# Kernel optimization log

Hardware: AMD Instinct MI355X
Metric: run time of the kernel (lower is better)

The kernel has to match this reference:

```python
import jax, jax.numpy as jnp
import numpy as np
import math

B, S, D = 2, 2048, 512
N_BUCKETS = 64
N_HYP = int(math.log2(N_BUCKETS))  # 6


def setup_inputs() -> dict:
    key = jax.random.key(0)
    ks = jax.random.split(key, 6)
    x = jax.random.normal(ks[0], (B, S, D), dtype=jnp.float32)
    # torch.nn.Linear params: weight [out,in], bias [out]
    Wq = jax.random.normal(ks[1], (D, D), dtype=jnp.float32) / jnp.sqrt(D)
    bq = jax.random.normal(ks[2], (D,), dtype=jnp.float32) * 0.01
    Wv = jax.random.normal(ks[3], (D, D), dtype=jnp.float32) / jnp.sqrt(D)
    bv = jax.random.normal(ks[4], (D,), dtype=jnp.float32) * 0.01
    hyperplanes = jax.random.normal(ks[5], (D + 1, N_HYP), dtype=jnp.float32)
    return {"x": x, "Wq": Wq, "bq": bq, "Wv": Wv, "bv": bv, "hyperplanes": hyperplanes}


def _get_buckets(q, hyperplanes):
    # append constant-1 feature: [B,S,D+1]
    qa = jnp.concatenate([q, jnp.ones(q.shape[:2] + (1,), q.dtype)], axis=2)
    proj = jnp.einsum('bse,en->bsn', qa, hyperplanes)
    bits = (proj >= 0).astype(jnp.float32)
    powers = (2.0 ** jnp.arange(N_HYP)).astype(jnp.float32)
    return jnp.einsum('bsn,n->bs', bits, powers)  # [B,S] float bucket ids


def reference(x, Wq, bq, Wv, bv, hyperplanes):
    q = x @ Wq.T + bq
    v = x @ Wv.T + bv
    buckets = _get_buckets(q, hyperplanes)  # [B,S]
    scale = 1.0 / math.sqrt(D)

    def body(acc, i):
        # NOTE: faithful to source: tokens IN bucket i are zeroed (masked_fill
        # with mask = buckets == i), then full dense softmax attention.
        mask = (buckets == i)[..., None]  # [B,S,1]
        qb = jnp.where(mask, 0.0, q)
        vb = jnp.where(mask, 0.0, v)
        att = jax.nn.softmax(jnp.einsum('bsd,btd->bst', qb, qb) * scale, axis=-1)
        return acc + jnp.einsum('bst,btd->bsd', att, vb), None

    init = jnp.zeros_like(x)
    out, _ = jax.lax.scan(body, init, jnp.arange(N_BUCKETS, dtype=jnp.float32))
    return out
```

## Files before the change

kernel.cpp:

```cpp
#include <hip/hip_runtime.h>
#include <math.h>

#define B_ 2
#define S_ 2048
#define D_ 512
#define NB_ 64
#define NH_ 6
#define ROWS (B_*S_)
#define SCALE 0.044194173824159216f

typedef float f32x4 __attribute__((ext_vector_type(4)));
typedef __bf16 bf16v8 __attribute__((ext_vector_type(8)));
typedef short s16x8 __attribute__((ext_vector_type(8)));
typedef unsigned short u16x4 __attribute__((ext_vector_type(4)));

__device__ __forceinline__ float b2f(unsigned short u) {
    unsigned int v = (unsigned int)u << 16;
    float f; __builtin_memcpy(&f, &v, 4); return f;
}
__device__ __forceinline__ unsigned short f2b(float f) {
    unsigned int v; __builtin_memcpy(&v, &f, 4);
    v += 0x7fffu + ((v >> 16) & 1u);
    return (unsigned short)(v >> 16);
}

#define GLOAD16(g, l) __builtin_amdgcn_global_load_lds( \
    (const __attribute__((address_space(1))) unsigned int*)(g), \
    (__attribute__((address_space(3))) unsigned int*)(uintptr_t)(l), 16, 0, 0)

__global__ void prep_kernel(
    const float* __restrict__ x, unsigned short* __restrict__ xh,
    const float* __restrict__ Wq, const float* __restrict__ Wv,
    unsigned short* __restrict__ Wqvh,
    float* __restrict__ Mrow, int* __restrict__ cnt, float* __restrict__ sumVall)
{
    int t = blockIdx.x * 256 + threadIdx.x;
    int stride = gridDim.x * 256;
    for (int i = t; i < ROWS * D_ / 4; i += stride) {
        float4 f = ((const float4*)x)[i];
        u16x4 u = { f2b(f.x), f2b(f.y), f2b(f.z), f2b(f.w) };
        ((u16x4*)xh)[i] = u;
    }
    for (int i = t; i < D_ * D_ / 4; i += stride) {
        float4 f = ((const float4*)Wq)[i];
        u16x4 u = { f2b(f.x), f2b(f.y), f2b(f.z), f2b(f.w) };
        ((u16x4*)Wqvh)[i] = u;
        float4 g = ((const float4*)Wv)[i];
        u16x4 w = { f2b(g.x), f2b(g.y), f2b(g.z), f2b(g.w) };
        ((u16x4*)(Wqvh + (size_t)D_ * D_))[i] = w;
    }
    for (int i = t; i < ROWS; i += stride) Mrow[i] = 0.f;
    for (int i = t; i < B_ * NB_; i += stride) cnt[i] = 0;
    for (int i = t; i < B_ * D_; i += stride) sumVall[i] = 0.f;
}

__global__ __launch_bounds__(256) void mfma_proj(
    const unsigned short* __restrict__ A, const unsigned short* __restrict__ B,
    const float* __restrict__ bq, const float* __restrict__ bv,
    float* __restrict__ MrowRaw, unsigned short* __restrict__ qh,
    float* __restrict__ v)
{
    __shared__ unsigned short Als[128 * 64];
    __shared__ unsigned short Bls[64 * 64];
    const int K = D_;
    int tid = threadIdx.x;
    int w = tid >> 6, l = tid & 63;
    int wr = w >> 1, wc = w & 1;

    int gx = gridDim.x;
    int nwg = gx * gridDim.y;
    int lin = blockIdx.y * gx + blockIdx.x;
    int qq = nwg >> 3;
    int wg = (lin & 7) * qq + (lin >> 3);
    int m0 = (wg / gx) * 128, n0 = (wg % gx) * 64;

    const unsigned short* asrc[4];
    #pragma unroll
    for (int j = 0; j < 4; ++j) {
        int chunk = w * 4 + j;
        int r = chunk * 8 + (l >> 3);
        asrc[j] = A + (size_t)(m0 + r) * K + ((l & 7) ^ (l >> 3)) * 8;
    }
    const unsigned short* bsrc[2];
    #pragma unroll
    for (int j = 0; j < 2; ++j) {
        int chunk = w * 2 + j;
        int r = n0 + chunk * 8 + (l >> 3);
        bsrc[j] = B + (size_t)r * K + ((l & 7) ^ (l >> 3)) * 8;
    }

    f32x4 acc[4][2] = {};
    int rl = l & 15, hi = l >> 4;

    for (int k0 = 0; k0 < K; k0 += 64) {
        #pragma unroll
        for (int j = 0; j < 4; ++j) GLOAD16(asrc[j] + k0, Als + (w * 4 + j) * 512);
        #pragma unroll
        for (int j = 0; j < 2; ++j) GLOAD16(bsrc[j] + k0, Bls + (w * 2 + j) * 512);
        __syncthreads();
        bf16v8 af[4][2], bfr[2][2];
        const char* Ab = (const char*)Als;
        const char* Bb = (const char*)Bls;
        #pragma unroll
        for (int kk = 0; kk < 2; ++kk) {
            int kb = kk * 64 + hi * 16;
            #pragma unroll
            for (int f = 0; f < 4; ++f) {
                int ra = wr * 64 + f * 16 + rl;
                af[f][kk] = *(const bf16v8*)(Ab + ra * 128 + (kb ^ ((ra & 7) << 4)));
            }
            #pragma unroll
            for (int f = 0; f < 2; ++f) {
                int rb = wc * 32 + f * 16 + rl;
                bfr[f][kk] = *(const bf16v8*)(Bb + rb * 128 + (kb ^ ((rb & 7) << 4)));
            }
        }
        #pragma unroll
        for (int fm = 0; fm < 4; ++fm)
            #pragma unroll
            for (int fn = 0; fn < 2; ++fn)
                #pragma unroll
                for (int kk = 0; kk < 2; ++kk)
                    acc[fm][fn] = __builtin_amdgcn_mfma_f32_16x16x32_bf16(
                        af[fm][kk], bfr[fn][kk], acc[fm][fn], 0, 0, 0);
        __syncthreads();
    }

    int colBase = n0 + wc * 32;
    if (colBase < D_) {
        #pragma unroll
        for (int fm = 0; fm < 4; ++fm) {
            float p[4] = {0.f, 0.f, 0.f, 0.f};
            #pragma unroll
            for (int fn = 0; fn < 2; ++fn) {
                int col = colBase + fn * 16 + rl;
                float bs = bq[col];
                #pragma unroll
                for (int r = 0; r < 4; ++r) {
                    int row = m0 + wr * 64 + fm * 16 + hi * 4 + r;
                    float cv = acc[fm][fn][r] + bs;
                    unsigned short h = f2b(cv);
                    qh[(size_t)row * D_ + col] = h;
                    float qb = b2f(h);
                    p[r] = fmaf(qb, qb, p[r]);
                }
            }
            #pragma unroll
            for (int mask = 1; mask < 16; mask <<= 1)
                #pragma unroll
                for (int r = 0; r < 4; ++r) p[r] += __shfl_xor(p[r], mask);
            if (rl == 0) {
                #pragma unroll
                for (int r = 0; r < 4; ++r) {
                    int row = m0 + wr * 64 + fm * 16 + hi * 4 + r;
                    atomicAdd(&MrowRaw[row], p[r]);
                }
            }
        }
    } else {
        #pragma unroll
        for (int fm = 0; fm < 4; ++fm)
            #pragma unroll
            for (int fn = 0; fn < 2; ++fn) {
                int col = colBase + fn * 16 + rl - D_;
                float bs = bv[col];
                #pragma unroll
                for (int r = 0; r < 4; ++r) {
                    int row = m0 + wr * 64 + fm * 16 + hi * 4 + r;
                    v[(size_t)row * D_ + col] = acc[fm][fn][r] + bs;
                }
            }
    }
}

__global__ __launch_bounds__(256) void mfma_qk(
    const unsigned short* __restrict__ qh, const int* __restrict__ prm,
    const float* __restrict__ Mrow, unsigned short* __restrict__ Eh)
{
    __shared__ unsigned short Als[128 * 64];
    __shared__ unsigned short Bls[128 * 64];
    const int K = D_;
    int tid = threadIdx.x;
    int w = tid >> 6, l = tid & 63;
    int wr = w >> 1, wc = w & 1;
    int zb = blockIdx.z;
    const unsigned short* A = qh + (size_t)zb * S_ * D_;
    prm += (size_t)zb * S_;
    const float* Mb = Mrow + (size_t)zb * S_;
    unsigned short* Eb = Eh + (size_t)zb * S_ * S_;

    int gx = gridDim.x;
    int nwg = gx * gridDim.y;
    int lin = blockIdx.y * gx + blockIdx.x;
    int qq = nwg >> 3;
    int wg = (lin & 7) * qq + (lin >> 3);
    int m0 = (wg / gx) * 128, n0 = (wg % gx) * 128;

    const unsigned short* asrc[4];
    const unsigned short* bsrc[4];
    #pragma unroll
    for (int j = 0; j < 4; ++j) {
        int chunk = w * 4 + j;
        int r = chunk * 8 + (l >> 3);
        int c = ((l & 7) ^ (l >> 3)) * 8;
        asrc[j] = A + (size_t)(m0 + r) * K + c;
        bsrc[j] = A + (size_t)prm[n0 + r] * K + c;
    }

    f32x4 acc[4][4] = {};
    int rl = l & 15, hi = l >> 4;

    for (int k0 = 0; k0 < K; k0 += 64) {
        #pragma unroll
        for (int j = 0; j < 4; ++j) GLOAD16(asrc[j] + k0, Als + (w * 4 + j) * 512);
        #pragma unroll
        for (int j = 0; j < 4; ++j) GLOAD16(bsrc[j] + k0, Bls + (w * 4 + j) * 512);
        __syncthreads();
        bf16v8 af[4][2], bfr[4][2];
        const char* Ab = (const char*)Als;
        const char* Bb = (const char*)Bls;
        #pragma unroll
        for (int kk = 0; kk < 2; ++kk) {
            int kb = kk * 64 + hi * 16;
            #pragma unroll
            for (int f = 0; f < 4; ++f) {
                int ra = wr * 64 + f * 16 + rl;
                af[f][kk] = *(const bf16v8*)(Ab + ra * 128 + (kb ^ ((ra & 7) << 4)));
                int rb = wc * 64 + f * 16 + rl;
                bfr[f][kk] = *(const bf16v8*)(Bb + rb * 128 + (kb ^ ((rb & 7) << 4)));
            }
        }
        #pragma unroll
        for (int fm = 0; fm < 4; ++fm)
            #pragma unroll
            for (int fn = 0; fn < 4; ++fn)
                #pragma unroll
                for (int kk = 0; kk < 2; ++kk)
                    acc[fm][fn] = __builtin_amdgcn_mfma_f32_16x16x32_bf16(
                        af[fm][kk], bfr[fn][kk], acc[fm][fn], 0, 0, 0);
        __syncthreads();
    }

    #pragma unroll
    for (int fm = 0; fm < 4; ++fm) {
        #pragma unroll
        for (int r = 0; r < 4; ++r) {
            int row = m0 + wr * 64 + fm * 16 + hi * 4 + r;
            float m = Mb[row];
            #pragma unroll
            for (int fn = 0; fn < 4; ++fn) {
                int col = n0 + wc * 64 + fn * 16 + rl;
                float ev = __expf(fmaf(acc[fm][fn][r], SCALE, -m));
                Eb[(size_t)row * S_ + col] = f2b(ev);
            }
        }
    }
}

__global__ __launch_bounds__(256) void mfma_pv64(
    const unsigned short* __restrict__ Eh, const unsigned short* __restrict__ vT,
    const float* __restrict__ sumVall, const float* __restrict__ sumVb,
    const int* __restrict__ bucket, float* __restrict__ out)
{
    __shared__ unsigned short Als[64 * 64];
    __shared__ unsigned short Bls[64 * 64];
    int tid = threadIdx.x, w = tid >> 6, l = tid & 63;
    int wr = w >> 1, wc = w & 1, rl = l & 15, hi = l >> 4;
    int zb = blockIdx.z;
    const unsigned short* A  = Eh + (size_t)zb * S_ * S_;
    const unsigned short* Bv = vT + (size_t)zb * D_ * S_;
    const float* sva = sumVall + (size_t)zb * D_;
    const float* svb = sumVb + (size_t)zb * NB_ * D_;
    const int* bkt = bucket + (size_t)zb * S_;
    float* outb = out + (size_t)zb * S_ * D_;

    int lin = blockIdx.y * 8 + blockIdx.x;
    int xcd = lin & 7, rest = lin >> 3;
    int m0 = (((rest >> 3) << 3) | xcd) * 64;
    int n0 = (rest & 7) * 64;

    const unsigned short* asrc[2];
    const unsigned short* bsrc[2];
    #pragma unroll
    for (int j = 0; j < 2; ++j) {
        int chunk = w * 2 + j;
        int r = chunk * 8 + (l >> 3);
        int c = ((l & 7) ^ (l >> 3)) * 8;
        asrc[j] = A  + (size_t)(m0 + r) * S_ + c;
        bsrc[j] = Bv + (size_t)(n0 + r) * S_ + c;
    }

    f32x4 acc[2][2] = {};
    for (int k0 = 0; k0 < S_; k0 += 64) {
        #pragma unroll
        for (int j = 0; j < 2; ++j) GLOAD16(asrc[j] + k0, Als + (w * 2 + j) * 512);
        #pragma unroll
        for (int j = 0; j < 2; ++j) GLOAD16(bsrc[j] + k0, Bls + (w * 2 + j) * 512);
        __syncthreads();
        bf16v8 af[2][2], bfr[2][2];
        const char* Ab = (const char*)Als;
        const char* Bb = (const char*)Bls;
        #pragma unroll
        for (int kk = 0; kk < 2; ++kk) {
            int kb = kk * 64 + hi * 16;
            #pragma unroll
            for (int f = 0; f < 2; ++f) {
                int ra = wr * 32 + f * 16 + rl;
                af[f][kk] = *(const bf16v8*)(Ab + ra * 128 + (kb ^ ((ra & 7) << 4)));
                int rb = wc * 32 + f * 16 + rl;
                bfr[f][kk] = *(const bf16v8*)(Bb + rb * 128 + (kb ^ ((rb & 7) << 4)));
            }
        }
        #pragma unroll
        for (int fm = 0; fm < 2; ++fm)
            #pragma unroll
            for (int fn = 0; fn < 2; ++fn)
                #pragma unroll
                for (int kk = 0; kk < 2; ++kk)
                    acc[fm][fn] = __builtin_amdgcn_mfma_f32_16x16x32_bf16(
                        af[fm][kk], bfr[fn][kk], acc[fm][fn], 0, 0, 0);
        __syncthreads();
    }
    const float invS = 1.0f / (float)S_;
    #pragma unroll
    for (int fm = 0; fm < 2; ++fm)
        #pragma unroll
        for (int fn = 0; fn < 2; ++fn) {
            int col = n0 + wc * 32 + fn * 16 + rl;
            float sa = sva[col];
            #pragma unroll
            for (int r = 0; r < 4; ++r) {
                int row = m0 + wr * 32 + fm * 16 + hi * 4 + r;
                int bm = bkt[row];
                outb[(size_t)row * D_ + col] =
                    acc[fm][fn][r] + (sa - svb[(size_t)bm * D_ + col]) * invS;
            }
        }
}

__global__ __launch_bounds__(256) void vprep_kernel(
    const float* __restrict__ v, const int* __restrict__ perm,
    unsigned short* __restrict__ vT,
    const int* __restrict__ cnt, const int* __restrict__ idxl,
    float* __restrict__ sumVb, float* __restrict__ sumVall)
{
    int bid = blockIdx.x;
    if (bid < 2048) {
        __shared__ float tl[32][33];
        int b = bid >> 10;
        int r = bid & 1023;
        int d0 = (r & 15) * 32, s0 = (r >> 4) * 32;
        int tx = threadIdx.x & 31, ty = threadIdx.x >> 5;
        const float* vb = v + (size_t)b * S_ * D_;
        const int* pm = perm + (size_t)b * S_;
        #pragma unroll
        for (int i = 0; i < 4; ++i)
            tl[ty + i * 8][tx] = vb[(size_t)pm[s0 + ty + i * 8] * D_ + d0 + tx];
        __syncthreads();
        unsigned short* vt = vT + (size_t)b * D_ * S_;
        #pragma unroll
        for (int i = 0; i < 4; ++i)
            vt[(size_t)(d0 + ty + i * 8) * S_ + s0 + tx] = f2b(tl[tx][ty + i * 8]);
    } else {
        int sid = bid - 2048;
        int j = sid & 63, b = (sid >> 6) & 1, dblk = sid >> 7;
        int d = dblk * 256 + threadIdx.x;
        int n = cnt[b * NB_ + j];
        const int* lst = idxl + ((size_t)(b * NB_ + j)) * S_;
        const float* vb = v + (size_t)b * S_ * D_;
        float acc = 0.f;
        for (int k = 0; k < n; ++k)
            acc += vb[(size_t)lst[k] * D_ + d];
        sumVb[((size_t)b * NB_ + j) * D_ + d] = acc;
        atomicAdd(&sumVall[b * D_ + d], acc);
    }
}

__global__ __launch_bounds__(64) void bucket_kernel(
    const unsigned short* __restrict__ qh, const float* __restrict__ H,
    int* __restrict__ bucket, float* __restrict__ Mrow,
    int* __restrict__ cnt, int* __restrict__ idxl)
{
    int row = blockIdx.x;
    int lane = threadIdx.x;
    const unsigned short* qr = qh + (size_t)row * D_;
    float proj[NH_] = {};
    s16x8 qv8 = *(const s16x8*)(qr + lane * 8);
    #pragma unroll
    for (int i = 0; i < 8; ++i) {
        float qv = b2f((unsigned short)qv8[i]);
        int d = lane * 8 + i;
        #pragma unroll
        for (int n = 0; n < NH_; ++n)
            proj[n] = fmaf(qv, H[d * NH_ + n], proj[n]);
    }
    #pragma unroll
    for (int off = 32; off; off >>= 1) {
        #pragma unroll
        for (int n = 0; n < NH_; ++n) proj[n] += __shfl_down(proj[n], off);
    }
    if (lane == 0) {
        int bk = 0;
        #pragma unroll
        for (int n = 0; n < NH_; ++n) {
            float p = proj[n] + H[D_ * NH_ + n];
            if (p >= 0.f) bk |= (1 << n);
        }
        bucket[row] = bk;
        Mrow[row] = Mrow[row] * SCALE;
        int b = row >> 11, s = row & (S_ - 1);
        int pos = atomicAdd(&cnt[b * NB_ + bk], 1);
        idxl[((size_t)(b * NB_ + bk)) * S_ + pos] = s;
    }
}

__global__ __launch_bounds__(256) void permprefix_kernel(
    const int* __restrict__ cnt, const int* __restrict__ idxl,
    int* __restrict__ off, int* __restrict__ perm, int* __restrict__ p2b)
{
    int b = blockIdx.x;
    int tid = threadIdx.x;
    __shared__ int offs[NB_ + 1];
    if (tid < 64) {
        int c = cnt[b * NB_ + tid];
        int x = c;
        #pragma unroll
        for (int o = 1; o < 64; o <<= 1) {
            int y = __shfl_up(x, o);
            if (tid >= o) x += y;
        }
        offs[tid] = x - c;
        off[b * (NB_ + 1) + tid] = x - c;
        if (tid == 63) { offs[64] = x; off[b * (NB_ + 1) + 64] = x; }
    }
    __syncthreads();
    int j = tid >> 2, sub = tid & 3;
    int o = offs[j];
    int c2 = offs[j + 1] - o;
    const int* lst = idxl + ((size_t)(b * NB_ + j)) * S_;
    for (int k = sub; k < c2; k += 4) {
        perm[(size_t)b * S_ + o + k] = lst[k];
        p2b[(size_t)b * S_ + o + k] = j;
    }
}

__global__ __launch_bounds__(256) void zwgamma_kernel(
    unsigned short* __restrict__ Eh, const int* __restrict__ p2b,
    const int* __restrict__ off, const int* __restrict__ cnt,
    const int* __restrict__ bucket, const float* __restrict__ Mrow)
{
    int row = blockIdx.x;
    int b = row >> 11;
    __shared__ float er[S_];
    __shared__ float zl[NB_];
    __shared__ float wl[NB_ + 1];
    int tid = threadIdx.x;
    unsigned short* Er = Eh + (size_t)row * S_;
    int t0 = tid * 8;
    s16x8 ev = *(const s16x8*)(Er + t0);
    #pragma unroll
    for (int i = 0; i < 8; ++i)
        er[t0 + i] = b2f((unsigned short)ev[i]);
    __syncthreads();
    {
        int j = tid >> 2, sub = tid & 3;
        int lo = off[b * (NB_ + 1) + j], hiX = off[b * (NB_ + 1) + j + 1];
        float z = 0.f;
        for (int k = lo + sub; k < hiX; k += 4) z += er[k];
        z += __shfl_xor(z, 1);
        z += __shfl_xor(z, 2);
        if (sub == 0) zl[j] = z;
    }
    __syncthreads();
    if (tid < NB_) {
        int j = tid;
        float zj = zl[j];
        float ztot = zj;
        #pragma unroll
        for (int o = 32; o; o >>= 1) ztot += __shfl_xor(ztot, o);
        int bs = bucket[row];
        float em = __expf(-Mrow[row]);
        float wj = 0.f;
        if (j != bs) wj = 1.0f / (ztot - zj + (float)cnt[b * NB_ + j] * em);
        float Wt = wj;
        #pragma unroll
        for (int o = 32; o; o >>= 1) Wt += __shfl_xor(Wt, o);
        wl[j] = wj;
        if (j == 0) wl[NB_] = Wt;
    }
    __syncthreads();
    float Wt = wl[NB_];
    const int* pb = p2b + (size_t)b * S_ + t0;
    int4 b0 = *(const int4*)pb;
    int4 b1 = *(const int4*)(pb + 4);
    s16x8 ov;
    ov[0] = (short)f2b(er[t0 + 0] * (Wt - wl[b0.x]));
    ov[1] = (short)f2b(er[t0 + 1] * (Wt - wl[b0.y]));
    ov[2] = (short)f2b(er[t0 + 2] * (Wt - wl[b0.z]));
    ov[3] = (short)f2b(er[t0 + 3] * (Wt - wl[b0.w]));
    ov[4] = (short)f2b(er[t0 + 4] * (Wt - wl[b1.x]));
    ov[5] = (short)f2b(er[t0 + 5] * (Wt - wl[b1.y]));
    ov[6] = (short)f2b(er[t0 + 6] * (Wt - wl[b1.z]));
    ov[7] = (short)f2b(er[t0 + 7] * (Wt - wl[b1.w]));
    *(s16x8*)(Er + t0) = ov;
}

extern "C" void kernel_launch(void* const* d_in, const int* in_sizes, int n_in,
                              void* d_out, int out_size, void* d_ws, size_t ws_size,
                              hipStream_t stream) {
    (void)in_sizes; (void)n_in; (void)out_size; (void)ws_size;
    const float* x  = (const float*)d_in[0];
    const float* Wq = (const float*)d_in[1];
    const float* bq = (const float*)d_in[2];
    const float* Wv = (const float*)d_in[3];
    const float* bv = (const float*)d_in[4];
    const float* H  = (const float*)d_in[5];
    float* out = (float*)d_out;

    char* p = (char*)d_ws;
    auto alloc = [&](size_t bytes) -> char* {
        char* r = p; p += (bytes + 255) & ~(size_t)255; return r;
    };
    float* v       = (float*)alloc((size_t)ROWS * D_ * 4);
    float* Mrow    = (float*)alloc((size_t)ROWS * 4);
    float* sumVb   = (float*)alloc((size_t)B_ * NB_ * D_ * 4);
    float* sumVall = (float*)alloc((size_t)B_ * D_ * 4);
    int*   bucket  = (int*)alloc((size_t)ROWS * 4);
    int*   cnt     = (int*)alloc((size_t)B_ * NB_ * 4);
    int*   offb    = (int*)alloc((size_t)B_ * (NB_ + 1) * 4);
    int*   perm    = (int*)alloc((size_t)B_ * S_ * 4);
    int*   p2b     = (int*)alloc((size_t)B_ * S_ * 4);
    int*   idxl    = (int*)alloc((size_t)B_ * NB_ * S_ * 4);
    unsigned short* xh   = (unsigned short*)alloc((size_t)ROWS * D_ * 2);
    unsigned short* qh   = (unsigned short*)alloc((size_t)ROWS * D_ * 2);
    unsigned short* Wqvh = (unsigned short*)alloc((size_t)2 * D_ * D_ * 2);
    unsigned short* vTh  = (unsigned short*)alloc((size_t)B_ * D_ * S_ * 2);
    unsigned short* Eh   = (unsigned short*)alloc((size_t)B_ * S_ * S_ * 2);

    prep_kernel<<<2048, 256, 0, stream>>>(x, xh, Wq, Wv, Wqvh, Mrow, cnt, sumVall);
    mfma_proj<<<dim3(2 * D_ / 64, ROWS / 128, 1), 256, 0, stream>>>(
        xh, Wqvh, bq, bv, Mrow, qh, v);
    bucket_kernel<<<ROWS, 64, 0, stream>>>(qh, H, bucket, Mrow, cnt, idxl);
    permprefix_kernel<<<B_, 256, 0, stream>>>(cnt, idxl, offb, perm, p2b);
    vprep_kernel<<<2048 + 256, 256, 0, stream>>>(v, perm, vTh, cnt, idxl, sumVb, sumVall);
    mfma_qk<<<dim3(S_ / 128, S_ / 128, B_), 256, 0, stream>>>(qh, perm, Mrow, Eh);
    zwgamma_kernel<<<ROWS, 256, 0, stream>>>(Eh, p2b, offb, cnt, bucket, Mrow);
    mfma_pv64<<<dim3(D_ / 64, S_ / 64, B_), 256, 0, stream>>>(
        Eh, vTh, sumVall, sumVb, bucket, out);
}
```

Baseline: 106.5 us.

## Fuse per-row bucket weighting into PV GEMM, dropping zwgamma pass

Removes the separate zwgamma kernel, which read and rewrote the full bf16 E matrix. The PV GEMM block now computes per-row bucket sums and weights itself and scales E tiles in registers before writing them to LDS. This avoids one full read-modify-write of E (2x2048x2048 bf16). In exchange, each of the 8 n-column blocks redundantly rereads its 64 E rows for the bucket sums, and the A tile is now loaded through registers instead of direct-to-LDS loads.

```diff
diff --git a/kernel.cpp b/kernel.cpp
--- a/kernel.cpp
+++ b/kernel.cpp
@@ -257,21 +257,28 @@
     }
 }
 
-__global__ __launch_bounds__(256) void mfma_pv64(
+__global__ __launch_bounds__(256) void mfma_pvzw(
     const unsigned short* __restrict__ Eh, const unsigned short* __restrict__ vT,
+    const int* __restrict__ p2b, const int* __restrict__ offb,
+    const int* __restrict__ cnt, const int* __restrict__ bucket,
+    const float* __restrict__ Mrow,
     const float* __restrict__ sumVall, const float* __restrict__ sumVb,
-    const int* __restrict__ bucket, float* __restrict__ out)
-{
-    __shared__ unsigned short Als[64 * 64];
-    __shared__ unsigned short Bls[64 * 64];
+    float* __restrict__ out)
+{
+    __shared__ float ZorA[4096];
+    __shared__ float wl[64][NB_ + 1];
+    __shared__ int off_l[NB_ + 1];
     int tid = threadIdx.x, w = tid >> 6, l = tid & 63;
     int wr = w >> 1, wc = w & 1, rl = l & 15, hi = l >> 4;
     int zb = blockIdx.z;
     const unsigned short* A  = Eh + (size_t)zb * S_ * S_;
     const unsigned short* Bv = vT + (size_t)zb * D_ * S_;
+    const int* pbg = p2b + (size_t)zb * S_;
+    const int* cntb = cnt + zb * NB_;
+    const int* bkt = bucket + (size_t)zb * S_;
+    const float* Mb = Mrow + (size_t)zb * S_;
     const float* sva = sumVall + (size_t)zb * D_;
     const float* svb = sumVb + (size_t)zb * NB_ * D_;
-    const int* bkt = bucket + (size_t)zb * S_;
     float* outb = out + (size_t)zb * S_ * D_;
 
     int lin = blockIdx.y * 8 + blockIdx.x;
@@ -279,27 +286,121 @@
     int m0 = (((rest >> 3) << 3) | xcd) * 64;
     int n0 = (rest & 7) * 64;
 
-    const unsigned short* asrc[2];
+    if (tid <= NB_) off_l[tid] = offb[zb * (NB_ + 1) + tid];
+    #pragma unroll
+    for (int i = 0; i < 16; ++i) ZorA[tid * 16 + i] = 0.f;
+    __syncthreads();
+    {
+        int r = tid >> 2, sub = tid & 3;
+        const unsigned short* Er = A + (size_t)(m0 + r) * S_ + sub * 512;
+        int j = pbg[sub * 512];
+        float run = 0.f;
+        for (int t = 0; t < 512; t += 8) {
+            s16x8 ev = *(const s16x8*)(Er + t);
+            int tg = sub * 512 + t;
+            if (tg + 8 <= off_l[j + 1]) {
+                run += b2f((unsigned short)ev[0]) + b2f((unsigned short)ev[1])
+                     + b2f((unsigned short)ev[2]) + b2f((unsigned short)ev[3])
+                     + b2f((unsigned short)ev[4]) + b2f((unsigned short)ev[5])
+                     + b2f((unsigned short)ev[6]) + b2f((unsigned short)ev[7]);
+            } else {
+                #pragma unroll
+                for (int i = 0; i < 8; ++i) {
+                    int tgi = tg + i;
+                    while (j < NB_ - 1 && tgi >= off_l[j + 1]) {
+                        atomicAdd(&ZorA[r * 64 + j], run); run = 0.f; ++j;
+                    }
+                    run += b2f((unsigned short)ev[i]);
+                }
+            }
+        }
+        atomicAdd(&ZorA[r * 64 + j], run);
+    }
+    __syncthreads();
+    {
+        for (int it = 0; it < 16; ++it) {
+            int rr = (w << 4) + it;
+            float zj = ZorA[rr * 64 + l];
+            float ztot = zj;
+            #pragma unroll
+            for (int o = 32; o; o >>= 1) ztot += __shfl_xor(ztot, o);
+            int row = m0 + rr;
+            float em = __expf(-Mb[row]);
+            int bs = bkt[row];
+            float wj = 0.f;
+            if (l != bs) wj = 1.0f / (ztot - zj + (float)cntb[l] * em);
+            float Wt = wj;
+            #pragma unroll
+            for (int o = 32; o; o >>= 1) Wt += __shfl_xor(Wt, o);
+            wl[rr][l] = wj;
+            if (l == 0) wl[rr][NB_] = Wt;
+        }
+    }
+    __syncthreads();
+
+    unsigned short* AlsB = (unsigned short*)ZorA;
+    unsigned short* BlsB = AlsB + 64 * 64;
+
+    int rA[2]; float wtA[2];
+    const unsigned short* asrc2[2];
+    #pragma unroll
+    for (int j = 0; j < 2; ++j) {
+        rA[j] = (w * 2 + j) * 8 + (l >> 3);
+        wtA[j] = wl[rA[j]][NB_];
+        asrc2[j] = A + (size_t)(m0 + rA[j]) * S_ + (l & 7) * 8;
+    }
     const unsigned short* bsrc[2];
     #pragma unroll
     for (int j = 0; j < 2; ++j) {
         int chunk = w * 2 + j;
         int r = chunk * 8 + (l >> 3);
-        int c = ((l & 7) ^ (l >> 3)) * 8;
-        asrc[j] = A  + (size_t)(m0 + r) * S_ + c;
-        bsrc[j] = Bv + (size_t)(n0 + r) * S_ + c;
-    }
+        bsrc[j] = Bv + (size_t)(n0 + r) * S_ + ((l & 7) ^ (l >> 3)) * 8;
+    }
+    const int* pbp = pbg + (l & 7) * 8;
+
+    s16x8 curA[2];
+    int4 curP0, curP1;
+    curA[0] = *(const s16x8*)(asrc2[0]);
+    curA[1] = *(const s16x8*)(asrc2[1]);
+    curP0 = *(const int4*)(pbp);
+    curP1 = *(const int4*)(pbp + 4);
 
     f32x4 acc[2][2] = {};
     for (int k0 = 0; k0 < S_; k0 += 64) {
         #pragma unroll
-        for (int j = 0; j < 2; ++j) GLOAD16(asrc[j] + k0, Als + (w * 2 + j) * 512);
-        #pragma unroll
-        for (int j = 0; j < 2; ++j) GLOAD16(bsrc[j] + k0, Bls + (w * 2 + j) * 512);
+        for (int j = 0; j < 2; ++j) GLOAD16(bsrc[j] + k0, BlsB + (w * 2 + j) * 512);
+        s16x8 nxtA[2]; int4 nxtP0, nxtP1;
+        int k1 = k0 + 64;
+        if (k1 < S_) {
+            nxtA[0] = *(const s16x8*)(asrc2[0] + k1);
+            nxtA[1] = *(const s16x8*)(asrc2[1] + k1);
+            nxtP0 = *(const int4*)(pbp + k1);
+            nxtP1 = *(const int4*)(pbp + k1 + 4);
+        }
+        #pragma unroll
+        for (int j = 0; j < 2; ++j) {
+            int r = rA[j];
+            float wt = wtA[j];
+            const float* wrow = &wl[r][0];
+            s16x8 o;
+            if (curP0.x == curP1.w) {
+                float g = wt - wrow[curP0.x];
+                #pragma unroll
+                for (int i = 0; i < 8; ++i)
+                    o[i] = (short)f2b(b2f((unsigned short)curA[j][i]) * g);
+            } else {
+                int bb[8] = {curP0.x, curP0.y, curP0.z, curP0.w,
+                             curP1.x, curP1.y, curP1.z, curP1.w};
+                #pragma unroll
+                for (int i = 0; i < 8; ++i)
+                    o[i] = (short)f2b(b2f((unsigned short)curA[j][i]) * (wt - wrow[bb[i]]));
+            }
+            *(s16x8*)((char*)AlsB + r * 128 + (((l & 7) ^ (r & 7)) << 4)) = o;
+        }
         __syncthreads();
         bf16v8 af[2][2], bfr[2][2];
-        const char* Ab = (const char*)Als;
-        const char* Bb = (const char*)Bls;
+        const char* Ab = (const char*)AlsB;
+        const char* Bb = (const char*)BlsB;
         #pragma unroll
         for (int kk = 0; kk < 2; ++kk) {
             int kb = kk * 64 + hi * 16;
@@ -320,6 +421,8 @@
                     acc[fm][fn] = __builtin_amdgcn_mfma_f32_16x16x32_bf16(
                         af[fm][kk], bfr[fn][kk], acc[fm][fn], 0, 0, 0);
         __syncthreads();
+        curA[0] = nxtA[0]; curA[1] = nxtA[1];
+        curP0 = nxtP0; curP1 = nxtP1;
     }
     const float invS = 1.0f / (float)S_;
     #pragma unroll
@@ -442,67 +545,6 @@
         perm[(size_t)b * S_ + o + k] = lst[k];
         p2b[(size_t)b * S_ + o + k] = j;
     }
-}
-
-__global__ __launch_bounds__(256) void zwgamma_kernel(
-    unsigned short* __restrict__ Eh, const int* __restrict__ p2b,
-    const int* __restrict__ off, const int* __restrict__ cnt,
-    const int* __restrict__ bucket, const float* __restrict__ Mrow)
-{
-    int row = blockIdx.x;
-    int b = row >> 11;
-    __shared__ float er[S_];
-    __shared__ float zl[NB_];
-    __shared__ float wl[NB_ + 1];
-    int tid = threadIdx.x;
-    unsigned short* Er = Eh + (size_t)row * S_;
-    int t0 = tid * 8;
-    s16x8 ev = *(const s16x8*)(Er + t0);
-    #pragma unroll
-    for (int i = 0; i < 8; ++i)
-        er[t0 + i] = b2f((unsigned short)ev[i]);
-    __syncthreads();
-    {
-        int j = tid >> 2, sub = tid & 3;
-        int lo = off[b * (NB_ + 1) + j], hiX = off[b * (NB_ + 1) + j + 1];
-        float z = 0.f;
-        for (int k = lo + sub; k < hiX; k += 4) z += er[k];
-        z += __shfl_xor(z, 1);
-        z += __shfl_xor(z, 2);
-        if (sub == 0) zl[j] = z;
-    }
-    __syncthreads();
-    if (tid < NB_) {
-        int j = tid;
-        float zj = zl[j];
-        float ztot = zj;
-        #pragma unroll
-        for (int o = 32; o; o >>= 1) ztot += __shfl_xor(ztot, o);
-        int bs = bucket[row];
-        float em = __expf(-Mrow[row]);
-        float wj = 0.f;
-        if (j != bs) wj = 1.0f / (ztot - zj + (float)cnt[b * NB_ + j] * em);
-        float Wt = wj;
-        #pragma unroll
-        for (int o = 32; o; o >>= 1) Wt += __shfl_xor(Wt, o);
-        wl[j] = wj;
-        if (j == 0) wl[NB_] = Wt;
-    }
-    __syncthreads();
-    float Wt = wl[NB_];
-    const int* pb = p2b + (size_t)b * S_ + t0;
-    int4 b0 = *(const int4*)pb;
-    int4 b1 = *(const int4*)(pb + 4);
-    s16x8 ov;
-    ov[0] = (short)f2b(er[t0 + 0] * (Wt - wl[b0.x]));
-    ov[1] = (short)f2b(er[t0 + 1] * (Wt - wl[b0.y]));
-    ov[2] = (short)f2b(er[t0 + 2] * (Wt - wl[b0.z]));
-    ov[3] = (short)f2b(er[t0 + 3] * (Wt - wl[b0.w]));
-    ov[4] = (short)f2b(er[t0 + 4] * (Wt - wl[b1.x]));
-    ov[5] = (short)f2b(er[t0 + 5] * (Wt - wl[b1.y]));
-    ov[6] = (short)f2b(er[t0 + 6] * (Wt - wl[b1.z]));
-    ov[7] = (short)f2b(er[t0 + 7] * (Wt - wl[b1.w]));
-    *(s16x8*)(Er + t0) = ov;
 }
 
 extern "C" void kernel_launch(void* const* d_in, const int* in_sizes, int n_in,
@@ -544,7 +586,6 @@
     permprefix_kernel<<<B_, 256, 0, stream>>>(cnt, idxl, offb, perm, p2b);
     vprep_kernel<<<2048 + 256, 256, 0, stream>>>(v, perm, vTh, cnt, idxl, sumVb, sumVall);
     mfma_qk<<<dim3(S_ / 128, S_ / 128, B_), 256, 0, stream>>>(qh, perm, Mrow, Eh);
-    zwgamma_kernel<<<ROWS, 256, 0, stream>>>(Eh, p2b, offb, cnt, bucket, Mrow);
-    mfma_pv64<<<dim3(D_ / 64, S_ / 64, B_), 256, 0, stream>>>(
-        Eh, vTh, sumVall, sumVb, bucket, out);
-}
+    mfma_pvzw<<<dim3(D_ / 64, S_ / 64, B_), 256, 0, stream>>>(
+        Eh, vTh, p2b, offb, cnt, bucket, Mrow, sumVall, sumVb, out);
+}
```

New measurement: 173.1 us. +62.5%, slower.
